# Kernel optimization log

Hardware: AMD Instinct MI355X
Metric: run time of the kernel (lower is better)

## Reference

```python
import jax, jax.numpy as jnp
import numpy as np

EPS = 1e-8          # torch nn.CosineSimilarity default eps
DIST_THR = 31.5     # 0.7 * 45 (module default)


def setup_inputs() -> dict:
    key = jax.random.key(0)
    k1, k2, k3, k4, k5 = jax.random.split(key, 5)
    B, C, H, W = 8, 256, 48, 48
    y = jax.random.normal(k1, (B, C, H, W), dtype=jnp.float32)
    yp = jax.random.normal(k2, (B, C, H, W), dtype=jnp.float32)
    z = jax.random.normal(k3, (B, C, H, W), dtype=jnp.float32)
    zp = jax.random.normal(k4, (B, C, H, W), dtype=jnp.float32)
    # distances in [0, 63): threshold 31.5 selects ~half of the pairs
    distances = jax.random.uniform(k5, (H, W, H, W), dtype=jnp.float32) * 63.0
    return {"y": y, "yp": yp, "z": z, "zp": zp, "distances": distances}


def _pairwise_cosine(a, b):
    # a, b: [B, C, N]; returns [B, N, N] cosine similarity over channel dim,
    # equivalent to CosineSimilarity(dim=1)(a[..., None], b[..., None, :])
    # but without materializing the [B, C, N, N] broadcast intermediate.
    dots = jnp.einsum('bcn,bcm->bnm', a, b)                       # [B,N,N]
    na = jnp.maximum(jnp.linalg.norm(a, axis=1), EPS)             # [B,N]
    nb = jnp.maximum(jnp.linalg.norm(b, axis=1), EPS)             # [B,N]
    return dots / (na[:, :, None] * nb[:, None, :])


def reference(y, yp, z, zp, distances):
    B, C = y.shape[0], y.shape[1]
    yf = y.reshape(B, C, -1)    # [B,C,N]
    ypf = yp.reshape(B, C, -1)
    zf = z.reshape(B, C, -1)
    zpf = zp.reshape(B, C, -1)

    cos_y_zp = _pairwise_cosine(yf, zpf)   # [B,N,N]
    cos_yp_z = _pairwise_cosine(zf, ypf)   # [B,N,N]

    H1, W1, H2, W2 = distances.shape
    mask = (distances.reshape(H1 * W1, H2 * W2) < DIST_THR)       # [N,N]

    # masked_select with mask broadcast over batch, then mean:
    # mean over B * count(mask) selected elements of -(cos1 + cos2)
    s = jnp.sum(jnp.where(mask[None, :, :], cos_y_zp + cos_yp_z, 0.0))
    cnt = jnp.sum(mask).astype(s.dtype) * B
    return -s / cnt
```

## Files before the change

kernel.cpp:

```cpp
#include <hip/hip_runtime.h>
#include <stdint.h>

#define GLOBAL_AS __attribute__((address_space(1)))
#define LDS_AS __attribute__((address_space(3)))

typedef _Float16 half_t;
typedef _Float16 f16x8 __attribute__((ext_vector_type(8)));
typedef float f32x4 __attribute__((ext_vector_type(4)));

static constexpr int BATCH = 8;
static constexpr int CH = 256;
static constexpr int N = 2304;
static constexpr int KTOT = 4096;
static constexpr int MW = 72;
static constexpr int MWORDS = 165888;
static constexpr int LROW = 258;
static constexpr float EPS = 1e-8f;
static constexpr float THR = 31.5f;
static constexpr int NBLK = 243;


__global__ __launch_bounds__(256) void prep_kernel(
    const float* __restrict__ y, const float* __restrict__ yp,
    const float* __restrict__ z, const float* __restrict__ zp,
    const float* __restrict__ dist,
    half_t* __restrict__ At, half_t* __restrict__ Bt,
    uint32_t* __restrict__ maskw, unsigned int* __restrict__ c_part) {
  const int t = threadIdx.x;
  const int bz = blockIdx.z;

  if (bz >= 4) {
    const int blk = ((bz - 4) * 8 + blockIdx.y) * 36 + blockIdx.x;
    const int w = blk * 256 + t;
    int c = 0;
    if (w < MWORDS) {
      const float4* p = (const float4*)(dist + (size_t)w * 32);
      uint32_t bits = 0;
#pragma unroll
      for (int q = 0; q < 8; ++q) {
        float4 v = p[q];
        bits |= (v.x < THR ? 1u : 0u) << (q * 4);
        bits |= (v.y < THR ? 1u : 0u) << (q * 4 + 1);
        bits |= (v.z < THR ? 1u : 0u) << (q * 4 + 2);
        bits |= (v.w < THR ? 1u : 0u) << (q * 4 + 3);
      }
      maskw[w] = bits;
      c = __popc(bits);
    }
#pragma unroll
    for (int off = 32; off; off >>= 1) c += __shfl_down(c, off, 64);
    __shared__ int mred[4];
    if ((t & 63) == 0) mred[t >> 6] = c;
    __syncthreads();
    if (t == 0)
      c_part[blk] = (unsigned int)(mred[0] + mred[1] + mred[2] + mred[3]);
    return;
  }

  const int b = blockIdx.y;
  const int n0 = blockIdx.x * 64;
  const float* src; half_t* dst; int kh;
  switch (bz) {
    case 0:  src = y;  dst = At; kh = 0;    break;
    case 1:  src = z;  dst = At; kh = 2048; break;
    case 2:  src = zp; dst = Bt; kh = 0;    break;
    default: src = yp; dst = Bt; kh = 2048; break;
  }
  const int kbase = kh + b * 256;
  const int col4 = (t & 15) * 4;
  const int cb = t >> 4;

  const float* base = src + (size_t)(b * CH + cb * 16) * N + n0 + col4;
  float4 v[16];
#pragma unroll
  for (int i = 0; i < 16; ++i) v[i] = *(const float4*)(base + (size_t)i * N);

  float ss[4] = {0.f, 0.f, 0.f, 0.f};
#pragma unroll
  for (int i = 0; i < 16; ++i) {
    ss[0] = fmaf(v[i].x, v[i].x, ss[0]);
    ss[1] = fmaf(v[i].y, v[i].y, ss[1]);
    ss[2] = fmaf(v[i].z, v[i].z, ss[2]);
    ss[3] = fmaf(v[i].w, v[i].w, ss[3]);
  }
  __shared__ float partial[16][65];
  __shared__ float sc[64];
  __shared__ half_t tile[64 * LROW];
#pragma unroll
  for (int j = 0; j < 4; ++j) partial[cb][col4 + j] = ss[j];
  __syncthreads();
  if (t < 64) {
    float s = 0.f;
#pragma unroll
    for (int k = 0; k < 16; ++k) s += partial[k][t];
    sc[t] = 1.0f / fmaxf(sqrtf(s), EPS);
  }
  __syncthreads();

#pragma unroll
  for (int j = 0; j < 4; ++j) {
    const float scj = sc[col4 + j];
    union { half_t h[16]; f16x8 v2[2]; } u;
#pragma unroll
    for (int i = 0; i < 16; ++i)
      u.h[i] = (half_t)(((const float*)&v[i])[j] * scj);
    f16x8* q = (f16x8*)(tile + (col4 + j) * LROW + cb * 16);
    q[0] = u.v2[0];
    q[1] = u.v2[1];
  }
  __syncthreads();

  {
    const int r = t >> 4, c = t & 15;
#pragma unroll
    for (int p = 0; p < 4; ++p) {
      const int row = p * 16 + r;
      half_t* gout = dst + (size_t)(n0 + row) * KTOT + kbase;
      const half_t* lrow = tile + row * LROW;
#pragma unroll
      for (int inst = 0; inst < 2; ++inst) {
        const int off = c * 8 + inst * 128;
        *(f16x8*)(gout + off) = *(const f16x8*)(lrow + off);
      }
    }
  }
}

__global__ __launch_bounds__(512, 2) void gemm_kernel(
    const half_t* __restrict__ At, const half_t* __restrict__ Bt,
    const uint32_t* __restrict__ maskw, float* __restrict__ s_part) {
  __shared__ __align__(16) half_t As[4 * 8192];
  __shared__ __align__(16) half_t Bs[4 * 8192];
  __shared__ float red[8];

  const int t = threadIdx.x;
  const int lane = t & 63;
  const int w8 = t >> 6;

  const int orig = blockIdx.x;
  const int xcd = orig & 7;
  const int wid = (xcd < 3 ? xcd * 31 : 93 + (xcd - 3) * 30) + (orig >> 3);
  const int zt = wid / 81;
  const int t81 = wid % 81;
  const int n0 = (t81 / 9) * 256;
  const int m0 = (t81 % 9) * 256;
  const int k0 = zt * 1376;
  const int NT = 43 - (zt == 2);

  const int srow = t >> 2;
  const int schunk = ((t & 3) ^ ((srow >> 1) & 3)) * 8;
  const half_t* gA = At + (size_t)(n0 + srow) * KTOT + k0 + schunk;
  const half_t* gB = Bt + (size_t)(m0 + srow) * KTOT + k0 + schunk;

  auto stage = [&](int j) {
    const int buf = j & 3;
    const half_t* ga = gA + j * 32;
    const half_t* gb = gB + j * 32;
    half_t* la = As + buf * 8192 + w8 * 512;
    half_t* lb = Bs + buf * 8192 + w8 * 512;
    __builtin_amdgcn_global_load_lds((const GLOBAL_AS void*)ga, (LDS_AS void*)la, 16, 0, 0);
    __builtin_amdgcn_global_load_lds((const GLOBAL_AS void*)(ga + (size_t)128 * KTOT),
                                     (LDS_AS void*)(la + 128 * 32), 16, 0, 0);
    __builtin_amdgcn_global_load_lds((const GLOBAL_AS void*)gb, (LDS_AS void*)lb, 16, 0, 0);
    __builtin_amdgcn_global_load_lds((const GLOBAL_AS void*)(gb + (size_t)128 * KTOT),
                                     (LDS_AS void*)(lb + 128 * 32), 16, 0, 0);
  };

  const int fr = lane & 15;
  const int clog = lane >> 4;
  const int wA = w8 >> 2;
  const int wB = w8 & 3;
  const int ksw = (clog ^ ((fr >> 1) & 3)) * 8;
  const int aoff = (wA * 128 + fr) * 32 + ksw;
  const int boff = (wB * 64 + fr) * 32 + ksw;

  f32x4 acc[8][4] = {};

#define GEMM_TILE(KT, VMSTR, DO_STAGE)                                         \
  {                                                                            \
    asm volatile("s_waitcnt " VMSTR ::: "memory");                             \
    __builtin_amdgcn_s_barrier();                                              \
    asm volatile("" ::: "memory");                                             \
    if (DO_STAGE) stage((KT) + 3);                                             \
    const half_t* Ab = As + ((KT) & 3) * 8192;                                 \
    const half_t* Bb = Bs + ((KT) & 3) * 8192;                                 \
    f16x8 af[8], bf[4];                                                        \
    _Pragma("unroll") for (int j = 0; j < 4; ++j)                              \
        bf[j] = *(const f16x8*)(Bb + boff + j * 512);                          \
    _Pragma("unroll") for (int i = 0; i < 8; ++i)                              \
        af[i] = *(const f16x8*)(Ab + aoff + i * 512);                          \
    __builtin_amdgcn_s_setprio(1);                                             \
    _Pragma("unroll") for (int i = 0; i < 8; ++i)                              \
      _Pragma("unroll") for (int j = 0; j < 4; ++j)                            \
        acc[i][j] =                                                            \
            __builtin_amdgcn_mfma_f32_16x16x32_f16(af[i], bf[j], acc[i][j], 0, 0, 0); \
    __builtin_amdgcn_s_setprio(0);                                             \
  }

  stage(0); stage(1); stage(2);

  int kt = 0;
  for (; kt < NT - 3; ++kt) GEMM_TILE(kt, "vmcnt(8)", true);
  GEMM_TILE(kt, "vmcnt(8)", false); ++kt;
  GEMM_TILE(kt, "vmcnt(4)", false); ++kt;
  GEMM_TILE(kt, "vmcnt(0)", false);
#undef GEMM_TILE

  float local = 0.f;
  const int mw0 = (m0 + wB * 64) >> 5;
#pragma unroll
  for (int i = 0; i < 8; ++i) {
    const int ng = n0 + wA * 128 + i * 16 + clog * 4;
#pragma unroll
    for (int r = 0; r < 4; ++r) {
      const uint2 wv = *(const uint2*)(maskw + (size_t)(ng + r) * MW + mw0);
#pragma unroll
      for (int j = 0; j < 4; ++j) {
        const uint32_t ww = (j & 2) ? wv.y : wv.x;
        if ((ww >> (fr + ((j & 1) << 4))) & 1u) local += acc[i][j][r];
      }
    }
  }
#pragma unroll
  for (int off = 32; off; off >>= 1) local += __shfl_down(local, off, 64);
  if (lane == 0) red[w8] = local;
  __syncthreads();
  if (t == 0) {
    float s = 0.f;
#pragma unroll
    for (int k = 0; k < 8; ++k) s += red[k];
    s_part[orig] = s;
  }
}

__global__ void finalize_kernel(const float* __restrict__ s_part,
                                const unsigned int* __restrict__ c_part,
                                float* __restrict__ out) {
  const int t = threadIdx.x;
  float local = 0.f;
  for (int i = t; i < NBLK; i += 256) local += s_part[i];
  unsigned int clocal = 0;
  for (int i = t; i < 864; i += 256) clocal += c_part[i];
#pragma unroll
  for (int off = 32; off; off >>= 1) {
    local += __shfl_down(local, off, 64);
    clocal += __shfl_down(clocal, off, 64);
  }
  __shared__ float red[4];
  __shared__ unsigned int credu[4];
  if ((t & 63) == 0) { red[t >> 6] = local; credu[t >> 6] = clocal; }
  __syncthreads();
  if (t == 0) {
    const float s = red[0] + red[1] + red[2] + red[3];
    const float cnt = (float)(credu[0] + credu[1] + credu[2] + credu[3]);
    out[0] = -s / (cnt * (float)BATCH);
  }
}

extern "C" void kernel_launch(void* const* d_in, const int* in_sizes, int n_in,
                              void* d_out, int out_size, void* d_ws, size_t ws_size,
                              hipStream_t stream) {
  const float* y    = (const float*)d_in[0];
  const float* yp   = (const float*)d_in[1];
  const float* z    = (const float*)d_in[2];
  const float* zp   = (const float*)d_in[3];
  const float* dist = (const float*)d_in[4];
  float* out = (float*)d_out;

  char* ws = (char*)d_ws;
  float* s_part = (float*)ws;
  unsigned int* c_part = (unsigned int*)(ws + 8192);
  half_t* At = (half_t*)(ws + 16384);
  half_t* Bt = (half_t*)(ws + 16384 + 18874368);
  uint32_t* maskw = (uint32_t*)(ws + 16384 + 2 * 18874368);

  prep_kernel<<<dim3(36, 8, 7), 256, 0, stream>>>(y, yp, z, zp, dist, At, Bt, maskw, c_part);
  gemm_kernel<<<dim3(NBLK), 512, 0, stream>>>(At, Bt, maskw, s_part);
  finalize_kernel<<<1, 256, 0, stream>>>(s_part, c_part, out);
}
```

Before: 182.6 us.

## Software-pipeline LDS fragment reads across k-tiles with double-buffered registers

Splits each k-tile's MFMA work into two halves and, between them, issues the LDS reads of the next tile's B and first-half A fragments into a second register set, so LDS latency overlaps MFMA execution. The K split across the three z-slices is also rebalanced to 44/42/42 tiles so every slice has an even tile count for the two-way unrolled loop. This costs extra VGPRs for the second fragment set, which may pressure the 2-wave occupancy target. The barrier and wait logic is also restructured, with the wait count changing from vmcnt(8) to vmcnt(4).

```diff
diff --git a/kernel.cpp b/kernel.cpp
--- a/kernel.cpp
+++ b/kernel.cpp
@@ -144,8 +144,8 @@
   const int t81 = wid % 81;
   const int n0 = (t81 / 9) * 256;
   const int m0 = (t81 % 9) * 256;
-  const int k0 = zt * 1376;
-  const int NT = 43 - (zt == 2);
+  const int k0 = zt ? (1408 + (zt - 1) * 1344) : 0;
+  const int NT = zt ? 42 : 44;
 
   const int srow = t >> 2;
   const int schunk = ((t & 3) ^ ((srow >> 1) & 3)) * 8;
@@ -176,35 +176,59 @@
 
   f32x4 acc[8][4] = {};
 
-#define GEMM_TILE(KT, VMSTR, DO_STAGE)                                         \
+#define READ_A(dst, BUF, IBASE)                                                \
+  _Pragma("unroll") for (int i = 0; i < 4; ++i)                                \
+      dst[i] = *(const f16x8*)(As + (BUF) * 8192 + aoff + ((IBASE) + i) * 512);
+#define READ_B(dst, BUF)                                                       \
+  _Pragma("unroll") for (int j = 0; j < 4; ++j)                                \
+      dst[j] = *(const f16x8*)(Bs + (BUF) * 8192 + boff + j * 512);
+
+#define BODY(KT, CA, CB, NA, NB, VMSTR, DO_STAGE, DO_NEXT)                     \
   {                                                                            \
     asm volatile("s_waitcnt " VMSTR ::: "memory");                             \
     __builtin_amdgcn_s_barrier();                                              \
     asm volatile("" ::: "memory");                                             \
     if (DO_STAGE) stage((KT) + 3);                                             \
-    const half_t* Ab = As + ((KT) & 3) * 8192;                                 \
-    const half_t* Bb = Bs + ((KT) & 3) * 8192;                                 \
-    f16x8 af[8], bf[4];                                                        \
-    _Pragma("unroll") for (int j = 0; j < 4; ++j)                              \
-        bf[j] = *(const f16x8*)(Bb + boff + j * 512);                          \
-    _Pragma("unroll") for (int i = 0; i < 8; ++i)                              \
-        af[i] = *(const f16x8*)(Ab + aoff + i * 512);                          \
+    f16x8 afh[4];                                                              \
+    READ_A(afh, (KT) & 3, 4);                                                  \
     __builtin_amdgcn_s_setprio(1);                                             \
-    _Pragma("unroll") for (int i = 0; i < 8; ++i)                              \
+    _Pragma("unroll") for (int i = 0; i < 4; ++i)                              \
       _Pragma("unroll") for (int j = 0; j < 4; ++j)                            \
         acc[i][j] =                                                            \
-            __builtin_amdgcn_mfma_f32_16x16x32_f16(af[i], bf[j], acc[i][j], 0, 0, 0); \
+            __builtin_amdgcn_mfma_f32_16x16x32_f16(CA[i], CB[j], acc[i][j], 0, 0, 0); \
     __builtin_amdgcn_s_setprio(0);                                             \
+    if (DO_NEXT) {                                                             \
+      READ_B(NB, ((KT) + 1) & 3);                                              \
+      READ_A(NA, ((KT) + 1) & 3, 0);                                           \
+    }                                                                          \
+    __builtin_amdgcn_s_setprio(1);                                             \
+    _Pragma("unroll") for (int i = 0; i < 4; ++i)                              \
+      _Pragma("unroll") for (int j = 0; j < 4; ++j)                            \
+        acc[4 + i][j] =                                                        \
+            __builtin_amdgcn_mfma_f32_16x16x32_f16(afh[i], CB[j], acc[4 + i][j], 0, 0, 0); \
+    __builtin_amdgcn_s_setprio(0);                                             \
   }
 
   stage(0); stage(1); stage(2);
+  asm volatile("s_waitcnt vmcnt(8)" ::: "memory");
+  __builtin_amdgcn_s_barrier();
+  asm volatile("" ::: "memory");
+  f16x8 af0[4], bf0[4], af1[4], bf1[4];
+  READ_B(bf0, 0);
+  READ_A(af0, 0, 0);
 
   int kt = 0;
-  for (; kt < NT - 3; ++kt) GEMM_TILE(kt, "vmcnt(8)", true);
-  GEMM_TILE(kt, "vmcnt(8)", false); ++kt;
-  GEMM_TILE(kt, "vmcnt(4)", false); ++kt;
-  GEMM_TILE(kt, "vmcnt(0)", false);
-#undef GEMM_TILE
+  for (; kt < NT - 4; kt += 2) {
+    BODY(kt,     af0, bf0, af1, bf1, "vmcnt(4)", true, true);
+    BODY(kt + 1, af1, bf1, af0, bf0, "vmcnt(4)", true, true);
+  }
+  BODY(NT - 4, af0, bf0, af1, bf1, "vmcnt(4)", true,  true);
+  BODY(NT - 3, af1, bf1, af0, bf0, "vmcnt(4)", false, true);
+  BODY(NT - 2, af0, bf0, af1, bf1, "vmcnt(0)", false, true);
+  BODY(NT - 1, af1, bf1, af0, bf0, "vmcnt(0)", false, false);
+#undef BODY
+#undef READ_A
+#undef READ_B
 
   float local = 0.f;
   const int mw0 = (m0 + wB * 64) >> 5;
```

Result: faster. 178.5 us (-2.2%).

## Restructure GEMM mainloop into 64-wide K double buffer with interleaved staging

Applied to the files above, without the earlier changes.

Replaces the 4-stage 32-wide K ring buffer with a 2-buffer 64-wide K tile scheme. Global-to-LDS loads are split into fine-grained chunks interleaved between eight MFMA sub-phases, each separated by barriers. The LDS swizzle is changed to 8-chunk rows, and the split-K boundaries move to 1408. The aim is to hide load latency and cut per-tile sync overhead, at the cost of many more barriers and tighter buffer-reuse ordering.

```diff
diff --git a/kernel.cpp b/kernel.cpp
--- a/kernel.cpp
+++ b/kernel.cpp
@@ -129,8 +129,8 @@
 __global__ __launch_bounds__(512, 2) void gemm_kernel(
     const half_t* __restrict__ At, const half_t* __restrict__ Bt,
     const uint32_t* __restrict__ maskw, float* __restrict__ s_part) {
-  __shared__ __align__(16) half_t As[4 * 8192];
-  __shared__ __align__(16) half_t Bs[4 * 8192];
+  __shared__ __align__(16) half_t As[2 * 16384];
+  __shared__ __align__(16) half_t Bs[2 * 16384];
   __shared__ float red[8];
 
   const int t = threadIdx.x;
@@ -144,80 +144,131 @@
   const int t81 = wid % 81;
   const int n0 = (t81 / 9) * 256;
   const int m0 = (t81 % 9) * 256;
-  const int k0 = zt * 1376;
-  const int NT = 43 - (zt == 2);
-
-  const int srow = t >> 2;
-  const int schunk = ((t & 3) ^ ((srow >> 1) & 3)) * 8;
-  const half_t* gA = At + (size_t)(n0 + srow) * KTOT + k0 + schunk;
-  const half_t* gB = Bt + (size_t)(m0 + srow) * KTOT + k0 + schunk;
-
-  auto stage = [&](int j) {
-    const int buf = j & 3;
-    const half_t* ga = gA + j * 32;
-    const half_t* gb = gB + j * 32;
-    half_t* la = As + buf * 8192 + w8 * 512;
-    half_t* lb = Bs + buf * 8192 + w8 * 512;
-    __builtin_amdgcn_global_load_lds((const GLOBAL_AS void*)ga, (LDS_AS void*)la, 16, 0, 0);
-    __builtin_amdgcn_global_load_lds((const GLOBAL_AS void*)(ga + (size_t)128 * KTOT),
-                                     (LDS_AS void*)(la + 128 * 32), 16, 0, 0);
-    __builtin_amdgcn_global_load_lds((const GLOBAL_AS void*)gb, (LDS_AS void*)lb, 16, 0, 0);
-    __builtin_amdgcn_global_load_lds((const GLOBAL_AS void*)(gb + (size_t)128 * KTOT),
-                                     (LDS_AS void*)(lb + 128 * 32), 16, 0, 0);
+  const int k0 = zt * 1408;
+  const int NI = (zt == 2) ? 10 : 11;
+
+  const int srow = t >> 3;
+  const int schunk8 = ((t & 7) ^ (srow & 7)) * 8;
+  const half_t* gA = At + (size_t)(n0 + srow) * KTOT + k0 + schunk8;
+  const half_t* gB = Bt + (size_t)(m0 + srow) * KTOT + k0 + schunk8;
+  const int ldsw = w8 * 512;
+
+  auto SA = [&](int tl, int u, int buf) {
+    __builtin_amdgcn_global_load_lds(
+        (const GLOBAL_AS void*)(gA + (size_t)(u * 64) * KTOT + tl * 64),
+        (LDS_AS void*)(As + buf * 16384 + u * 4096 + ldsw), 16, 0, 0);
   };
+  auto SB = [&](int tl, int u, int buf) {
+    __builtin_amdgcn_global_load_lds(
+        (const GLOBAL_AS void*)(gB + (size_t)(u * 64) * KTOT + tl * 64),
+        (LDS_AS void*)(Bs + buf * 16384 + u * 4096 + ldsw), 16, 0, 0);
+  };
 
   const int fr = lane & 15;
-  const int clog = lane >> 4;
+  const int cl = lane >> 4;
+  const int e = lane & 7;
+  const int ksw0 = ((((cl ^ e) & 3)) | (e & 4)) * 8;
+  const int ksw1 = ksw0 ^ 32;
   const int wA = w8 >> 2;
   const int wB = w8 & 3;
-  const int ksw = (clog ^ ((fr >> 1) & 3)) * 8;
-  const int aoff = (wA * 128 + fr) * 32 + ksw;
-  const int boff = (wB * 64 + fr) * 32 + ksw;
+  const int aoff = (wA * 128 + fr) * 64;
+  const int boff = (wB * 64 + fr) * 64;
 
   f32x4 acc[8][4] = {};
-
-#define GEMM_TILE(KT, VMSTR, DO_STAGE)                                         \
+  f16x8 af[4], bf[4];
+
+#define RD_A(BUF, QA, KSW)                                                     \
+  _Pragma("unroll") for (int i = 0; i < 4; ++i)                                \
+      af[i] = *(const f16x8*)(As + (BUF) * 16384 + aoff + (QA) * 4096 +        \
+                              i * 1024 + (KSW));
+#define RD_B(BUF, KSW)                                                         \
+  _Pragma("unroll") for (int j = 0; j < 4; ++j)                                \
+      bf[j] = *(const f16x8*)(Bs + (BUF) * 16384 + boff + j * 1024 + (KSW));
+#define MM(QA)                                                                 \
+  __builtin_amdgcn_s_setprio(1);                                               \
+  _Pragma("unroll") for (int i = 0; i < 4; ++i)                                \
+    _Pragma("unroll") for (int j = 0; j < 4; ++j)                              \
+      acc[(QA) * 4 + i][j] = __builtin_amdgcn_mfma_f32_16x16x32_f16(           \
+          af[i], bf[j], acc[(QA) * 4 + i][j], 0, 0, 0);                        \
+  __builtin_amdgcn_s_setprio(0);
+#define BARMID                                                                 \
+  __builtin_amdgcn_s_barrier();                                                \
+  asm volatile("s_waitcnt lgkmcnt(0)" ::: "memory");
+#define BAREND __builtin_amdgcn_s_barrier();
+
+#define ITER(SN)                                                               \
   {                                                                            \
-    asm volatile("s_waitcnt " VMSTR ::: "memory");                             \
-    __builtin_amdgcn_s_barrier();                                              \
-    asm volatile("" ::: "memory");                                             \
-    if (DO_STAGE) stage((KT) + 3);                                             \
-    const half_t* Ab = As + ((KT) & 3) * 8192;                                 \
-    const half_t* Bb = Bs + ((KT) & 3) * 8192;                                 \
-    f16x8 af[8], bf[4];                                                        \
-    _Pragma("unroll") for (int j = 0; j < 4; ++j)                              \
-        bf[j] = *(const f16x8*)(Bb + boff + j * 512);                          \
-    _Pragma("unroll") for (int i = 0; i < 8; ++i)                              \
-        af[i] = *(const f16x8*)(Ab + aoff + i * 512);                          \
-    __builtin_amdgcn_s_setprio(1);                                             \
-    _Pragma("unroll") for (int i = 0; i < 8; ++i)                              \
-      _Pragma("unroll") for (int j = 0; j < 4; ++j)                            \
-        acc[i][j] =                                                            \
-            __builtin_amdgcn_mfma_f32_16x16x32_f16(af[i], bf[j], acc[i][j], 0, 0, 0); \
-    __builtin_amdgcn_s_setprio(0);                                             \
-  }
-
-  stage(0); stage(1); stage(2);
-
-  int kt = 0;
-  for (; kt < NT - 3; ++kt) GEMM_TILE(kt, "vmcnt(8)", true);
-  GEMM_TILE(kt, "vmcnt(8)", false); ++kt;
-  GEMM_TILE(kt, "vmcnt(4)", false); ++kt;
-  GEMM_TILE(kt, "vmcnt(0)", false);
-#undef GEMM_TILE
+    const int u = 2 * j + 1, t2 = 2 * j + 2, t3 = 2 * j + 3;                   \
+                                                             \
+    RD_A(0, 0, ksw0); RD_B(0, ksw0);                                           \
+    SA(u, 1, 1); SA(u, 3, 1);                                                  \
+    BARMID; MM(0); BAREND;                                                     \
+                                                             \
+    RD_A(0, 1, ksw0);                                                          \
+    SB(u, 0, 1); SB(u, 1, 1);                                                  \
+    BARMID; MM(1); BAREND;                                                     \
+                                                             \
+    RD_A(0, 0, ksw1); RD_B(0, ksw1);                                           \
+    SB(u, 2, 1); SB(u, 3, 1);                                                  \
+    BARMID; MM(0); BAREND;                                                     \
+                                               \
+    RD_A(0, 1, ksw1);                                                          \
+    if (SN) {                                                                  \
+      SA(t2, 0, 0); SA(t2, 2, 0);                                              \
+      asm volatile("s_waitcnt vmcnt(2)" ::: "memory");                         \
+    } else {                                                                   \
+      asm volatile("s_waitcnt vmcnt(0)" ::: "memory");                         \
+    }                                                                          \
+    BARMID; MM(1); BAREND;                                                     \
+                                                        \
+    RD_A(1, 0, ksw0); RD_B(1, ksw0);                                           \
+    if (SN) { SA(t2, 1, 0); SA(t2, 3, 0); }                                    \
+    BARMID; MM(0); BAREND;                                                     \
+                                                                       \
+    RD_A(1, 1, ksw0);                                                          \
+    if (SN) { SB(t2, 0, 0); SB(t2, 1, 0); }                                    \
+    BARMID; MM(1); BAREND;                                                     \
+                                                                       \
+    RD_A(1, 0, ksw1); RD_B(1, ksw1);                                           \
+    if (SN) { SB(t2, 2, 0); SB(t2, 3, 0); }                                    \
+    BARMID; MM(0); BAREND;                                                     \
+                                                        \
+    RD_A(1, 1, ksw1);                                                          \
+    if (SN) {                                                                  \
+      SA(t3, 0, 1); SA(t3, 2, 1);                                              \
+      asm volatile("s_waitcnt vmcnt(2)" ::: "memory");                         \
+    }                                                                          \
+    BARMID; MM(1); BAREND;                                                     \
+  }
+
+  SA(0, 0, 0); SA(0, 1, 0); SA(0, 2, 0); SA(0, 3, 0);
+  SB(0, 0, 0); SB(0, 1, 0); SB(0, 2, 0); SB(0, 3, 0);
+  SA(1, 0, 1); SA(1, 2, 1);
+  asm volatile("s_waitcnt vmcnt(2)" ::: "memory");
+  __builtin_amdgcn_s_barrier();
+
+  int j = 0;
+  for (; j < NI - 1; ++j) ITER(true);
+  ITER(false);
+#undef ITER
+#undef RD_A
+#undef RD_B
+#undef MM
+#undef BARMID
+#undef BAREND
 
   float local = 0.f;
   const int mw0 = (m0 + wB * 64) >> 5;
 #pragma unroll
   for (int i = 0; i < 8; ++i) {
-    const int ng = n0 + wA * 128 + i * 16 + clog * 4;
+    const int ng = n0 + wA * 128 + i * 16 + cl * 4;
 #pragma unroll
     for (int r = 0; r < 4; ++r) {
       const uint2 wv = *(const uint2*)(maskw + (size_t)(ng + r) * MW + mw0);
 #pragma unroll
-      for (int j = 0; j < 4; ++j) {
-        const uint32_t ww = (j & 2) ? wv.y : wv.x;
-        if ((ww >> (fr + ((j & 1) << 4))) & 1u) local += acc[i][j][r];
+      for (int j2 = 0; j2 < 4; ++j2) {
+        const uint32_t ww = (j2 & 2) ? wv.y : wv.x;
+        if ((ww >> (fr + ((j2 & 1) << 4))) & 1u) local += acc[i][j2][r];
       }
     }
   }
```

Measured after the change: 175.9 us. -3.6%, faster.
